# Optimization experiments

Measured on AMD Instinct MI355X. Metric: run time of the kernel, lower is better.

Reference implementation:

```python
import jax, jax.numpy as jnp
import numpy as np

B, C = 128, 1024
BN_EPS = 1e-5
LEAKY_SLOPE = 0.1


def setup_inputs() -> dict:
    key = jax.random.key(0)
    ks = jax.random.split(key, 8)
    visual_feat = jax.random.normal(ks[0], (B, C), dtype=jnp.float32)
    tactile_feat = jax.random.normal(ks[1], (B, C), dtype=jnp.float32)
    # ConvFuse: Conv2d(1024,1024,k=3,p=1) + BatchNorm2d(1024) (eval) + LeakyReLU(0.1)
    fan_in = C * 3 * 3
    conv_w = jax.random.normal(ks[2], (C, C, 3, 3), dtype=jnp.float32) / np.sqrt(fan_in)
    conv_b = jax.random.normal(ks[3], (C,), dtype=jnp.float32) * 0.01
    bn_gamma = jax.random.uniform(ks[4], (C,), dtype=jnp.float32, minval=0.5, maxval=1.5)
    bn_beta = jax.random.normal(ks[5], (C,), dtype=jnp.float32) * 0.1
    bn_mean = jax.random.normal(ks[6], (C,), dtype=jnp.float32) * 0.1
    bn_var = jax.random.uniform(ks[7], (C,), dtype=jnp.float32, minval=0.5, maxval=1.5)
    return {
        "visual_feat": visual_feat,
        "tactile_feat": tactile_feat,
        "conv_w": conv_w,
        "conv_b": conv_b,
        "bn_gamma": bn_gamma,
        "bn_beta": bn_beta,
        "bn_mean": bn_mean,
        "bn_var": bn_var,
    }


def reference(visual_feat, tactile_feat, conv_w, conv_b, bn_gamma, bn_beta, bn_mean, bn_var):
    # h1 = visual (B,C,1), h3 = tactile (B,C,1)
    # scores[b,i,j] = tactile[b,i] * visual[b,j]  -> (B,C,C)
    scores = tactile_feat[:, :, None] * visual_feat[:, None, :]
    attn = jax.nn.softmax(scores, axis=-1)
    # crossed[b,i] = sum_j attn[b,i,j] * visual[b,j]
    crossed = jnp.einsum("bij,bj->bi", attn, visual_feat)
    # residual add, reshape to (B,C,1,1)  (H = W = 1)
    h = (visual_feat + crossed)[:, :, None, None]
    # Dropout2d(0.3) in eval mode -> identity
    # Conv2d 3x3 stride 1 pad 1 on 1x1 spatial
    y = jax.lax.conv_general_dilated(
        h, conv_w, window_strides=(1, 1), padding=((1, 1), (1, 1)),
        dimension_numbers=("NCHW", "OIHW", "NCHW"))
    y = y + conv_b[None, :, None, None]
    # BatchNorm2d (eval, running stats)
    inv = bn_gamma / jnp.sqrt(bn_var + BN_EPS)
    y = (y - bn_mean[None, :, None, None]) * inv[None, :, None, None] + bn_beta[None, :, None, None]
    # LeakyReLU(0.1)
    return jnp.where(y > 0, y, LEAKY_SLOPE * y)
```

## Files before the change

kernel.cpp:

```cpp
#include <hip/hip_runtime.h>
#include <math.h>

constexpr int Bb = 128;
constexpr int Cc = 1024;
constexpr float BN_EPS = 1e-5f;
constexpr float SLOPE = 0.1f;
constexpr float LOG2E = 1.44269504088896340736f;

constexpr int   TTAB   = 256;
constexpr float SRANGE = 6.0f;

constexpr int KCH = 64;
constexpr int OT  = 32;
constexpr int KS  = Cc / KCH;
constexpr int NOT = Cc / OT;
constexpr int HSR = 132;

__device__ inline float fast_exp2(float x) {
#if __has_builtin(__builtin_amdgcn_exp2f)
    return __builtin_amdgcn_exp2f(x);
#else
    return exp2f(x);
#endif
}

__global__ __launch_bounds__(256) void table_kernel(
    const float* __restrict__ vis, float* __restrict__ ftab,
    unsigned int* __restrict__ cnt) {
    __shared__ float vs[Cc];
    const int b = blockIdx.y;
    const int tid = threadIdx.x;
    if (blockIdx.x == 0 && b == 0 && tid < NOT) cnt[tid] = 0u;
    ((float4*)vs)[tid] = ((const float4*)(vis + (size_t)b * Cc))[tid];
    __syncthreads();

    const int tg = blockIdx.x * 64 + (tid >> 2);
    const int l  = tid & 3;
    const float s  = -SRANGE + (2.f * SRANGE) * (float)tg * (1.f / (TTAB - 1));
    const float s2 = s * LOG2E;
    float num0 = 0.f, num1 = 0.f, den0 = 0.f, den1 = 0.f;
#pragma unroll 4
    for (int it = 0; it < Cc / 16; ++it) {
        float4 v4 = ((const float4*)vs)[it * 4 + l];
        float e0 = fast_exp2(s2 * v4.x);
        float e1 = fast_exp2(s2 * v4.y);
        float e2 = fast_exp2(s2 * v4.z);
        float e3 = fast_exp2(s2 * v4.w);
        den0 += e0 + e2;
        den1 += e1 + e3;
        num0 = fmaf(v4.x, e0, num0);
        num1 = fmaf(v4.y, e1, num1);
        num0 = fmaf(v4.z, e2, num0);
        num1 = fmaf(v4.w, e3, num1);
    }
    float num = num0 + num1, den = den0 + den1;
    num += __shfl_xor(num, 1); den += __shfl_xor(den, 1);
    num += __shfl_xor(num, 2); den += __shfl_xor(den, 2);
    if (l == 0) ftab[(size_t)b * TTAB + tg] = num / den;
}

__global__ __launch_bounds__(256) void gemm_fused_kernel(
    const float* __restrict__ conv_w, const float* __restrict__ vis,
    const float* __restrict__ tac, const float* __restrict__ ftab,
    float* __restrict__ part, unsigned int* __restrict__ cnt,
    const float* __restrict__ cb, const float* __restrict__ gamma,
    const float* __restrict__ beta, const float* __restrict__ mean,
    const float* __restrict__ var, float* __restrict__ out) {
    __shared__ float hs[KCH * HSR];
    __shared__ float wss[OT * KCH];
    __shared__ unsigned int lastflag;
    const int kidx = blockIdx.x, ot = blockIdx.y;
    const int k0 = kidx * KCH, o0 = ot * OT;
    const int tid = threadIdx.x;

    constexpr float TSCALE = (TTAB - 1) / (2.f * SRANGE);
#pragma unroll
    for (int r = 0; r < 8; ++r) {
        int slot = tid + 256 * r;
        int b = slot >> 4, i0 = slot & 15;
        const float* tacb = tac + (size_t)b * Cc + k0;
        const float* visb = vis + (size_t)b * Cc + k0;
        const float* tb = ftab + (size_t)b * TTAB;
#pragma unroll
        for (int c = 0; c < 4; ++c) {
            int i = i0 + 16 * c;
            float s = tacb[i];
            float u = (s + SRANGE) * TSCALE;
            int it = (int)floorf(u);
            it = min(max(it, 0), TTAB - 2);
            float fr = u - (float)it;
            float f0 = tb[it], f1 = tb[it + 1];
            hs[i * HSR + b] = visb[i] + fmaf(fr, f1 - f0, f0);
        }
    }
#pragma unroll
    for (int r = 0; r < (OT * KCH) / 256; ++r) {
        int flat = tid + 256 * r;
        int o = flat >> 6, i = flat & (KCH - 1);
        wss[flat] = conv_w[((size_t)(o0 + o) * Cc + (k0 + i)) * 9 + 4];
    }
    __syncthreads();

    const int b0 = (tid & 31) * 4;
    const int oo = (tid >> 5) * 4;
    float4 acc[4] = {{0,0,0,0},{0,0,0,0},{0,0,0,0},{0,0,0,0}};
    for (int ig = 0; ig < KCH / 4; ++ig) {
        float4 w4[4];
#pragma unroll
        for (int c = 0; c < 4; ++c)
            w4[c] = *(const float4*)(wss + (oo + c) * KCH + ig * 4);
#pragma unroll
        for (int k = 0; k < 4; ++k) {
            float4 h4 = *(const float4*)(hs + (ig * 4 + k) * HSR + b0);
            float w0 = k == 0 ? w4[0].x : k == 1 ? w4[0].y : k == 2 ? w4[0].z : w4[0].w;
            float w1 = k == 0 ? w4[1].x : k == 1 ? w4[1].y : k == 2 ? w4[1].z : w4[1].w;
            float w2 = k == 0 ? w4[2].x : k == 1 ? w4[2].y : k == 2 ? w4[2].z : w4[2].w;
            float w3 = k == 0 ? w4[3].x : k == 1 ? w4[3].y : k == 2 ? w4[3].z : w4[3].w;
            acc[0].x = fmaf(h4.x, w0, acc[0].x); acc[0].y = fmaf(h4.y, w0, acc[0].y);
            acc[0].z = fmaf(h4.z, w0, acc[0].z); acc[0].w = fmaf(h4.w, w0, acc[0].w);
            acc[1].x = fmaf(h4.x, w1, acc[1].x); acc[1].y = fmaf(h4.y, w1, acc[1].y);
            acc[1].z = fmaf(h4.z, w1, acc[1].z); acc[1].w = fmaf(h4.w, w1, acc[1].w);
            acc[2].x = fmaf(h4.x, w2, acc[2].x); acc[2].y = fmaf(h4.y, w2, acc[2].y);
            acc[2].z = fmaf(h4.z, w2, acc[2].z); acc[2].w = fmaf(h4.w, w2, acc[2].w);
            acc[3].x = fmaf(h4.x, w3, acc[3].x); acc[3].y = fmaf(h4.y, w3, acc[3].y);
            acc[3].z = fmaf(h4.z, w3, acc[3].z); acc[3].w = fmaf(h4.w, w3, acc[3].w);
        }
    }

    float* ptile = part + ((size_t)ot * KS + kidx) * (Bb * OT);
#pragma unroll
    for (int k = 0; k < 4; ++k) {
        float4 ro;
        ro.x = k == 0 ? acc[0].x : k == 1 ? acc[0].y : k == 2 ? acc[0].z : acc[0].w;
        ro.y = k == 0 ? acc[1].x : k == 1 ? acc[1].y : k == 2 ? acc[1].z : acc[1].w;
        ro.z = k == 0 ? acc[2].x : k == 1 ? acc[2].y : k == 2 ? acc[2].z : acc[2].w;
        ro.w = k == 0 ? acc[3].x : k == 1 ? acc[3].y : k == 2 ? acc[3].z : acc[3].w;
        *(float4*)(ptile + (size_t)(b0 + k) * OT + oo) = ro;
    }
    __syncthreads();

    if (tid == 0) {
        unsigned int old = __hip_atomic_fetch_add(
            &cnt[ot], 1u, __ATOMIC_ACQ_REL, __HIP_MEMORY_SCOPE_AGENT);
        lastflag = (old == KS - 1) ? 1u : 0u;
    }
    __syncthreads();
    if (lastflag) {
        const float* pbase = part + (size_t)ot * KS * (Bb * OT);
#pragma unroll
        for (int r = 0; r < 4; ++r) {
            int q = tid + 256 * r;
            int b = q >> 3, ol4 = q & 7;
            float4 sum = {0.f, 0.f, 0.f, 0.f};
            for (int k = 0; k < KS; ++k) {
                float4 v = *(const float4*)(pbase + (size_t)k * (Bb * OT) + b * OT + ol4 * 4);
                sum.x += v.x; sum.y += v.y; sum.z += v.z; sum.w += v.w;
            }
            int o4 = (o0 >> 2) + ol4;
            float4 g = ((const float4*)gamma)[o4], bt = ((const float4*)beta)[o4];
            float4 mu = ((const float4*)mean)[o4], vr = ((const float4*)var)[o4];
            float4 cbv = ((const float4*)cb)[o4];
            float4 y;
            y.x = (sum.x + cbv.x - mu.x) * (g.x * rsqrtf(vr.x + BN_EPS)) + bt.x;
            y.y = (sum.y + cbv.y - mu.y) * (g.y * rsqrtf(vr.y + BN_EPS)) + bt.y;
            y.z = (sum.z + cbv.z - mu.z) * (g.z * rsqrtf(vr.z + BN_EPS)) + bt.z;
            y.w = (sum.w + cbv.w - mu.w) * (g.w * rsqrtf(vr.w + BN_EPS)) + bt.w;
            y.x = y.x > 0.f ? y.x : SLOPE * y.x;
            y.y = y.y > 0.f ? y.y : SLOPE * y.y;
            y.z = y.z > 0.f ? y.z : SLOPE * y.z;
            y.w = y.w > 0.f ? y.w : SLOPE * y.w;
            ((float4*)(out + (size_t)b * Cc + o0))[ol4] = y;
        }
    }
}

extern "C" void kernel_launch(void* const* d_in, const int* in_sizes, int n_in,
                              void* d_out, int out_size, void* d_ws, size_t ws_size,
                              hipStream_t stream) {
    const float* vis   = (const float*)d_in[0];
    const float* tac   = (const float*)d_in[1];
    const float* cw    = (const float*)d_in[2];
    const float* cb    = (const float*)d_in[3];
    const float* gamma = (const float*)d_in[4];
    const float* beta  = (const float*)d_in[5];
    const float* mean  = (const float*)d_in[6];
    const float* var   = (const float*)d_in[7];
    float* out = (float*)d_out;

    float* ftab = (float*)d_ws;
    float* part = ftab + (size_t)Bb * TTAB;
    unsigned int* cnt = (unsigned int*)(part + (size_t)NOT * KS * Bb * OT);

    table_kernel<<<dim3(TTAB / 64, Bb), 256, 0, stream>>>(vis, ftab, cnt);
    gemm_fused_kernel<<<dim3(KS, NOT), 256, 0, stream>>>(
        cw, vis, tac, ftab, part, cnt, cb, gamma, beta, mean, var, out);
}
```

Baseline: 126.6 us.

## Precompute h and compact center conv weights in a prep kernel

The table kernel becomes a prep kernel. Each of its batch blocks builds the full 256-entry softmax table in shared memory and writes the interpolated h = vis + crossed row to workspace. Extra blocks copy the center tap of conv_w into a contiguous 1024x1024 matrix, so the GEMM kernel can load h and weights as float4 instead of strided scalar gathers with per-element table lookups. The cost is a second pass over the center weights (a strided read plus a 4 MB write and reread) in every call, and each table value is now computed by one thread looping over all 1024 elements instead of four threads sharing the work.

```diff
diff --git a/kernel.cpp b/kernel.cpp
--- a/kernel.cpp
+++ b/kernel.cpp
@@ -10,11 +10,14 @@
 constexpr int   TTAB   = 256;
 constexpr float SRANGE = 6.0f;
 
-constexpr int KCH = 64;
-constexpr int OT  = 32;
-constexpr int KS  = Cc / KCH;
-constexpr int NOT = Cc / OT;
-constexpr int HSR = 132;
+constexpr int KCH  = 64;
+constexpr int OT   = 32;
+constexpr int KS   = Cc / KCH;
+constexpr int NOT_ = Cc / OT;
+constexpr int HSR  = 132;
+
+constexpr int NEVAL = Bb;
+constexpr int NCOMP = (Cc * Cc) / 256;
 
 __device__ inline float fast_exp2(float x) {
 #if __has_builtin(__builtin_amdgcn_exp2f)
@@ -24,24 +27,29 @@
 #endif
 }
 
-__global__ __launch_bounds__(256) void table_kernel(
-    const float* __restrict__ vis, float* __restrict__ ftab,
-    unsigned int* __restrict__ cnt) {
+__global__ __launch_bounds__(256) void prep_kernel(
+    const float* __restrict__ vis, const float* __restrict__ tac,
+    const float* __restrict__ conv_w, float* __restrict__ h,
+    float* __restrict__ wc, unsigned int* __restrict__ cnt) {
+    const int blk = blockIdx.x, tid = threadIdx.x;
+    if (blk >= NEVAL) {
+        size_t q = (size_t)(blk - NEVAL) * 256 + tid;
+        wc[q] = conv_w[q * 9 + 4];
+        return;
+    }
     __shared__ float vs[Cc];
-    const int b = blockIdx.y;
-    const int tid = threadIdx.x;
-    if (blockIdx.x == 0 && b == 0 && tid < NOT) cnt[tid] = 0u;
+    __shared__ float tl[TTAB];
+    const int b = blk;
+    if (blk == 0 && tid < NOT_) cnt[tid] = 0u;
     ((float4*)vs)[tid] = ((const float4*)(vis + (size_t)b * Cc))[tid];
     __syncthreads();
 
-    const int tg = blockIdx.x * 64 + (tid >> 2);
-    const int l  = tid & 3;
-    const float s  = -SRANGE + (2.f * SRANGE) * (float)tg * (1.f / (TTAB - 1));
+    const float s  = -SRANGE + (2.f * SRANGE) * (float)tid * (1.f / (TTAB - 1));
     const float s2 = s * LOG2E;
     float num0 = 0.f, num1 = 0.f, den0 = 0.f, den1 = 0.f;
 #pragma unroll 4
-    for (int it = 0; it < Cc / 16; ++it) {
-        float4 v4 = ((const float4*)vs)[it * 4 + l];
+    for (int j4 = 0; j4 < Cc / 4; ++j4) {
+        float4 v4 = ((const float4*)vs)[j4];
         float e0 = fast_exp2(s2 * v4.x);
         float e1 = fast_exp2(s2 * v4.y);
         float e2 = fast_exp2(s2 * v4.z);
@@ -53,15 +61,33 @@
         num0 = fmaf(v4.z, e2, num0);
         num1 = fmaf(v4.w, e3, num1);
     }
-    float num = num0 + num1, den = den0 + den1;
-    num += __shfl_xor(num, 1); den += __shfl_xor(den, 1);
-    num += __shfl_xor(num, 2); den += __shfl_xor(den, 2);
-    if (l == 0) ftab[(size_t)b * TTAB + tg] = num / den;
+    tl[tid] = (num0 + num1) / (den0 + den1);
+    __syncthreads();
+
+    constexpr float TSC = (TTAB - 1) / (2.f * SRANGE);
+    float4 t4 = ((const float4*)(tac + (size_t)b * Cc))[tid];
+    float4 v4 = ((const float4*)vs)[tid];
+    float4 h4;
+    {
+        float sv[4] = {t4.x, t4.y, t4.z, t4.w};
+        float vv[4] = {v4.x, v4.y, v4.z, v4.w};
+        float hv[4];
+#pragma unroll
+        for (int k = 0; k < 4; ++k) {
+            float u = (sv[k] + SRANGE) * TSC;
+            int i0 = (int)floorf(u);
+            i0 = min(max(i0, 0), TTAB - 2);
+            float fr = u - (float)i0;
+            float f0 = tl[i0], f1 = tl[i0 + 1];
+            hv[k] = vv[k] + fmaf(fr, f1 - f0, f0);
+        }
+        h4.x = hv[0]; h4.y = hv[1]; h4.z = hv[2]; h4.w = hv[3];
+    }
+    ((float4*)(h + (size_t)b * Cc))[tid] = h4;
 }
 
 __global__ __launch_bounds__(256) void gemm_fused_kernel(
-    const float* __restrict__ conv_w, const float* __restrict__ vis,
-    const float* __restrict__ tac, const float* __restrict__ ftab,
+    const float* __restrict__ h, const float* __restrict__ wc,
     float* __restrict__ part, unsigned int* __restrict__ cnt,
     const float* __restrict__ cb, const float* __restrict__ gamma,
     const float* __restrict__ beta, const float* __restrict__ mean,
@@ -73,31 +99,22 @@
     const int k0 = kidx * KCH, o0 = ot * OT;
     const int tid = threadIdx.x;
 
-    constexpr float TSCALE = (TTAB - 1) / (2.f * SRANGE);
 #pragma unroll
     for (int r = 0; r < 8; ++r) {
         int slot = tid + 256 * r;
-        int b = slot >> 4, i0 = slot & 15;
-        const float* tacb = tac + (size_t)b * Cc + k0;
-        const float* visb = vis + (size_t)b * Cc + k0;
-        const float* tb = ftab + (size_t)b * TTAB;
-#pragma unroll
-        for (int c = 0; c < 4; ++c) {
-            int i = i0 + 16 * c;
-            float s = tacb[i];
-            float u = (s + SRANGE) * TSCALE;
-            int it = (int)floorf(u);
-            it = min(max(it, 0), TTAB - 2);
-            float fr = u - (float)it;
-            float f0 = tb[it], f1 = tb[it + 1];
-            hs[i * HSR + b] = visb[i] + fmaf(fr, f1 - f0, f0);
-        }
-    }
-#pragma unroll
-    for (int r = 0; r < (OT * KCH) / 256; ++r) {
-        int flat = tid + 256 * r;
-        int o = flat >> 6, i = flat & (KCH - 1);
-        wss[flat] = conv_w[((size_t)(o0 + o) * Cc + (k0 + i)) * 9 + 4];
+        int b = slot >> 4, c4 = slot & 15;
+        float4 h4 = *(const float4*)(h + (size_t)b * Cc + k0 + 4 * c4);
+        hs[(4 * c4 + 0) * HSR + b] = h4.x;
+        hs[(4 * c4 + 1) * HSR + b] = h4.y;
+        hs[(4 * c4 + 2) * HSR + b] = h4.z;
+        hs[(4 * c4 + 3) * HSR + b] = h4.w;
+    }
+#pragma unroll
+    for (int r = 0; r < 2; ++r) {
+        int slot = tid + 256 * r;
+        int o = slot >> 4, i4 = slot & 15;
+        *(float4*)(wss + o * KCH + 4 * i4) =
+            *(const float4*)(wc + (size_t)(o0 + o) * Cc + k0 + 4 * i4);
     }
     __syncthreads();
 
@@ -187,11 +204,12 @@
     const float* var   = (const float*)d_in[7];
     float* out = (float*)d_out;
 
-    float* ftab = (float*)d_ws;
-    float* part = ftab + (size_t)Bb * TTAB;
-    unsigned int* cnt = (unsigned int*)(part + (size_t)NOT * KS * Bb * OT);
-
-    table_kernel<<<dim3(TTAB / 64, Bb), 256, 0, stream>>>(vis, ftab, cnt);
-    gemm_fused_kernel<<<dim3(KS, NOT), 256, 0, stream>>>(
-        cw, vis, tac, ftab, part, cnt, cb, gamma, beta, mean, var, out);
-}
+    float* h    = (float*)d_ws;
+    float* wc   = h + (size_t)Bb * Cc;
+    float* part = wc + (size_t)Cc * Cc;
+    unsigned int* cnt = (unsigned int*)(part + (size_t)NOT_ * KS * Bb * OT);
+
+    prep_kernel<<<NEVAL + NCOMP, 256, 0, stream>>>(vis, tac, cw, h, wc, cnt);
+    gemm_fused_kernel<<<dim3(KS, NOT_), 256, 0, stream>>>(
+        h, wc, part, cnt, cb, gamma, beta, mean, var, out);
+}
```

Result: slower. 129.4 us (+2.2%).
